# Performance work log

Hardware: AMD Instinct MI355X
Metric: run time of the kernel (lower is better)

The kernel has to match this reference:

```python
import jax, jax.numpy as jnp
import numpy as np

H = 1024      # hidden_size
I = 2048      # intermediate_size
E = 32        # num_routed_experts
B, S = 4, 2048


def setup_inputs() -> dict:
    key = jax.random.key(0)
    ks = jax.random.split(key, 8)
    scale = 0.02
    inp = {
        "hidden_states": jax.random.normal(ks[0], (B, S, H), dtype=jnp.float32),
        # router gate: stored [H, E] so logits = x @ gate_w
        "gate_w": jax.random.normal(ks[1], (H, E), dtype=jnp.float32) * scale,
        # shared SwiGLU (num_shared_experts=1), weights stored [in, out]
        "shared_gate_w": jax.random.normal(ks[2], (H, I), dtype=jnp.float32) * scale,
        "shared_up_w": jax.random.normal(ks[3], (H, I), dtype=jnp.float32) * scale,
        "shared_down_w": jax.random.normal(ks[4], (I, H), dtype=jnp.float32) * scale,
        # routed grouped SwiGLU, weights stored [E, in, out] (matches GroupedLinear)
        "routed_gate_w": jax.random.normal(ks[5], (E, H, I), dtype=jnp.float32) * scale,
        "routed_up_w": jax.random.normal(ks[6], (E, H, I), dtype=jnp.float32) * scale,
        "routed_down_w": jax.random.normal(ks[7], (E, I, H), dtype=jnp.float32) * scale,
    }
    return inp


def _grouped_mm(a, w, group_sizes):
    # a: [T, in], w: [E, in, out], group_sizes: [E] int32 -> [T, out]
    return jax.lax.ragged_dot(a, w, group_sizes)


def _swiglu(x, gw, uw, dw):
    return (jax.nn.silu(x @ gw) * (x @ uw)) @ dw


def reference(hidden_states, gate_w, shared_gate_w, shared_up_w, shared_down_w,
              routed_gate_w, routed_up_w, routed_down_w):
    b, s, h = hidden_states.shape
    x = hidden_states.reshape(-1, h)                      # [T, H]

    # ---- shared expert ----
    shared_out = _swiglu(x, shared_gate_w, shared_up_w, shared_down_w)

    # ---- router: top-1 ----
    logits = x @ gate_w                                   # [T, E]
    topk_ids = jnp.argmax(logits, axis=-1)                # [T]
    topk_val = jnp.max(logits, axis=-1)                   # [T]
    scores = jax.nn.sigmoid(topk_val)[:, None]            # [T, 1]
    xs = x * scores                                       # scale tokens by router score

    # ---- dispatch: sort tokens by expert id ----
    tokens_per_expert = jnp.zeros((E,), jnp.int32).at[topk_ids].add(1)
    order = jnp.argsort(topk_ids)                         # token ids sorted by expert
    sorted_x = xs[order]                                  # [T, H]

    # ---- grouped SwiGLU experts ----
    g = _grouped_mm(sorted_x, routed_gate_w, tokens_per_expert)   # [T, I]
    u = _grouped_mm(sorted_x, routed_up_w, tokens_per_expert)     # [T, I]
    d = _grouped_mm(jax.nn.silu(g) * u, routed_down_w, tokens_per_expert)  # [T, H]

    # ---- combine: unsort back to token order ----
    inv = jnp.argsort(order)
    routed_out = d[inv]

    return (shared_out + routed_out).reshape(b, s, h)
```

## Files before the change

### kernel.cpp

```cpp
#include <hip/hip_runtime.h>
#include <stdint.h>
#include <stddef.h>

#define TOK 8192
#define H 1024
#define IDIM 2048
#define NE 32
#define BM 128
#define BK 64
#define MAX_TILES 96

typedef __attribute__((ext_vector_type(8))) short short8;
typedef __attribute__((ext_vector_type(4))) float f32x4;
typedef __attribute__((ext_vector_type(4))) float float4v;
typedef __attribute__((ext_vector_type(4))) unsigned int uint4v;


__device__ __forceinline__ unsigned short f2bf(float x) {
  unsigned u = __builtin_bit_cast(unsigned, x);
  u += 0x7fffu + ((u >> 16) & 1u);
  return (unsigned short)(u >> 16);
}

__device__ __forceinline__ unsigned cvtpk(float lo, float hi) {
  unsigned r;
  asm("v_cvt_pk_bf16_f32 %0, %1, %2" : "=v"(r) : "v"(lo), "v"(hi));
  return r;
}

__device__ __forceinline__ void gll16(const void* g, void* l) {
  __builtin_amdgcn_global_load_lds(
      (const __attribute__((address_space(1))) unsigned int*)g,
      (__attribute__((address_space(3))) unsigned int*)l, 16, 0, 0);
}

__device__ __forceinline__ f32x4 mfma16(short8 a, short8 b, f32x4 c) {
  return __builtin_amdgcn_mfma_f32_16x16x32_bf16(a, b, c, 0, 0, 0);
}


__global__ __launch_bounds__(256) void tconv_kernel(
    const float* __restrict__ src0, unsigned short* __restrict__ dst0,
    int K, int N)
{
  __shared__ float t[64][65];
  const size_t mat = (size_t)K * N;
  const float* src = src0 + (size_t)blockIdx.z * mat;
  unsigned short* dst = dst0 + (size_t)blockIdx.z * mat;
  const int k0 = blockIdx.x * 64, n0 = blockIdx.y * 64;
  const int tid = threadIdx.x;
  {
    const int r = tid >> 4;
    const int c = (tid & 15) * 4;
    #pragma unroll
    for (int i = 0; i < 4; ++i) {
      float4v v = *(const float4v*)(src + (size_t)(k0 + r + i * 16) * N + (n0 + c));
      t[r + i * 16][c + 0] = v[0];
      t[r + i * 16][c + 1] = v[1];
      t[r + i * 16][c + 2] = v[2];
      t[r + i * 16][c + 3] = v[3];
    }
  }
  __syncthreads();
  {
    const int n = tid >> 2;
    const int kc = (tid & 3) * 16;
    uint4v o0, o1;
    #pragma unroll
    for (int q = 0; q < 4; ++q) {
      o0[q] = cvtpk(t[kc + 2 * q][n],     t[kc + 2 * q + 1][n]);
      o1[q] = cvtpk(t[kc + 8 + 2 * q][n], t[kc + 8 + 2 * q + 1][n]);
    }
    unsigned short* dp = dst + (size_t)(n0 + n) * K + (k0 + kc);
    *(uint4v*)dp = o0;
    *(uint4v*)(dp + 8) = o1;
  }
}


__global__ __launch_bounds__(256) void router_kernel(
    const float* __restrict__ x, const float* __restrict__ gw,
    unsigned short* __restrict__ xbf, unsigned short* __restrict__ xsbf,
    int* __restrict__ expert_id, int* __restrict__ counts)
{
  __shared__ float xl[8 * H];
  __shared__ float plog[8][8][NE];
  __shared__ float sscore[8];
  const int tid = threadIdx.x;
  const long t0 = (long)blockIdx.x * 8;

  const float4v* src = (const float4v*)(x + t0 * H);
  float4v* dst = (float4v*)xl;
  #pragma unroll
  for (int i = 0; i < 8; ++i) dst[tid + i * 256] = src[tid + i * 256];
  __syncthreads();

  {
    const int e = tid & 31, c = tid >> 5;
    float acc[8] = {0, 0, 0, 0, 0, 0, 0, 0};
    const float* gp = gw + (c * 128) * NE + e;
    for (int h = 0; h < 128; ++h) {
      float g = gp[h * NE];
      const float* xr = xl + (c * 128 + h);
      #pragma unroll
      for (int tk = 0; tk < 8; ++tk) acc[tk] += xr[tk * H] * g;
    }
    #pragma unroll
    for (int tk = 0; tk < 8; ++tk) plog[c][tk][e] = acc[tk];
  }
  __syncthreads();
  {
    const int e = tid & 31, tok = tid >> 5;
    float lg = 0.f;
    #pragma unroll
    for (int c = 0; c < 8; ++c) lg += plog[c][tok][e];
    float m = lg; int be = e;
    #pragma unroll
    for (int mask = 16; mask >= 1; mask >>= 1) {
      float om = __shfl_xor(m, mask);
      int   oe = __shfl_xor(be, mask);
      if (om > m || (om == m && oe < be)) { m = om; be = oe; }
    }
    if (e == 0) {
      sscore[tok] = 1.f / (1.f + __expf(-m));
      expert_id[t0 + tok] = be;
      atomicAdd(&counts[be], 1);
    }
  }
  __syncthreads();
  {
    const float sc = sscore[tid >> 5];
    const int base = (tid >> 5) * H + (tid & 31) * 32;
    #pragma unroll
    for (int i = 0; i < 4; ++i) {
      uint4v vx, vs;
      #pragma unroll
      for (int q = 0; q < 4; ++q) {
        const float a = xl[base + i * 8 + 2 * q];
        const float b = xl[base + i * 8 + 2 * q + 1];
        vx[q] = cvtpk(a, b);
        vs[q] = cvtpk(a * sc, b * sc);
      }
      *(uint4v*)(xbf  + t0 * H + base + i * 8) = vx;
      *(uint4v*)(xsbf + t0 * H + base + i * 8) = vs;
    }
  }
}


__global__ void scan_kernel(const int* __restrict__ counts, int* __restrict__ offsets,
                            int* __restrict__ cursor, int* __restrict__ tile_e,
                            int* __restrict__ tile_p, int* __restrict__ n_tiles)
{
  if (threadIdx.x != 0) return;
  int off = 0, nt = 0;
  for (int e = 0; e < NE; ++e) {
    offsets[e] = off; cursor[e] = off;
    int cc = counts[e];
    for (int k = 0; k < cc; k += BM) { tile_e[nt] = e; tile_p[nt] = off + k; ++nt; }
    off += cc;
  }
  offsets[NE] = off;
  n_tiles[0] = nt;
}


__global__ __launch_bounds__(256) void perm_kernel(
    const int* __restrict__ expert_id, int* __restrict__ cursor, int* __restrict__ perm)
{
  int t = blockIdx.x * 256 + threadIdx.x;
  int e = expert_id[t];
  int pos = atomicAdd(&cursor[e], 1);
  perm[pos] = t;
}


__global__ __launch_bounds__(256, 2) void gu_kernel(
    const unsigned short* __restrict__ xbf,
    const unsigned short* __restrict__ xsbf,
    const unsigned short* __restrict__ SG, const unsigned short* __restrict__ SU,
    const unsigned short* __restrict__ RG, const unsigned short* __restrict__ RU,
    unsigned short* __restrict__ act_sh, unsigned short* __restrict__ act_rt,
    const int* __restrict__ perm, const int* __restrict__ tile_e,
    const int* __restrict__ tile_p, const int* __restrict__ offsets,
    const int* __restrict__ n_tiles)
{
  __shared__ short Al[BM * BK];
  __shared__ short Gl[128 * BK];
  __shared__ short Ul[128 * BK];

  const int tid = threadIdx.x;
  const int wave = tid >> 6, lane = tid & 63;
  const int wm = wave >> 1, wn = wave & 1;

  const int bidx = blockIdx.y;
  const bool routed = bidx >= (TOK / BM);
  int row0, row_end;
  const unsigned short *Gt, *Ut, *A;
  unsigned short* act;
  if (routed) {
    const int tx = bidx - TOK / BM;
    if (tx >= *n_tiles) return;
    const int e = tile_e[tx];
    row0 = tile_p[tx];
    row_end = offsets[e + 1];
    Gt = RG + (size_t)e * H * IDIM;
    Ut = RU + (size_t)e * H * IDIM;
    A = xsbf; act = act_rt;
  } else {
    row0 = bidx * BM; row_end = row0 + BM;
    Gt = SG; Ut = SU;
    A = xbf; act = act_sh;
  }
  const int n0 = blockIdx.x * 128;

  const unsigned short *asrc[4], *gsrc[4], *usrc[4];
  int soff[4];
  #pragma unroll
  for (int i = 0; i < 4; ++i) {
    const int r = wave * 32 + i * 8 + (lane >> 3);
    int p = row0 + r;
    if (routed && p >= row_end) p = row0;
    const int arow = routed ? perm[p] : p;
    const int cb = ((lane & 7) * 16) ^ ((r & 7) << 4);
    asrc[i] = A  + (size_t)arow * H + (cb >> 1);
    gsrc[i] = Gt + (size_t)(n0 + r) * H + (cb >> 1);
    usrc[i] = Ut + (size_t)(n0 + r) * H + (cb >> 1);
    soff[i] = (wave * 32 + i * 8) * BK;
  }

  f32x4 accg[4][4] = {};
  f32x4 accu[4][4] = {};

  #pragma unroll 1
  for (int kt = 0; kt < H / BK; ++kt) {
    __syncthreads();
    #pragma unroll
    for (int i = 0; i < 4; ++i) gll16(asrc[i] + kt * BK, Al + soff[i]);
    #pragma unroll
    for (int i = 0; i < 4; ++i) gll16(gsrc[i] + kt * BK, Gl + soff[i]);
    #pragma unroll
    for (int i = 0; i < 4; ++i) gll16(usrc[i] + kt * BK, Ul + soff[i]);
    __syncthreads();

    #pragma unroll
    for (int kk = 0; kk < 2; ++kk) {
      short8 af[4];
      #pragma unroll
      for (int m = 0; m < 4; ++m) {
        const int r = wm * 64 + m * 16 + (lane & 15);
        const int cb = (kk * 64 + ((lane >> 4) * 16)) ^ ((r & 7) << 4);
        af[m] = *(const short8*)((const char*)Al + r * 128 + cb);
      }
      #pragma unroll
      for (int nf = 0; nf < 4; ++nf) {
        const int n = wn * 64 + nf * 16 + (lane & 15);
        const int cb = (kk * 64 + ((lane >> 4) * 16)) ^ ((n & 7) << 4);
        short8 bg = *(const short8*)((const char*)Gl + n * 128 + cb);
        short8 bu = *(const short8*)((const char*)Ul + n * 128 + cb);
        #pragma unroll
        for (int m = 0; m < 4; ++m) {
          accg[m][nf] = mfma16(af[m], bg, accg[m][nf]);
          accu[m][nf] = mfma16(af[m], bu, accu[m][nf]);
        }
      }
    }
  }

  #pragma unroll
  for (int m = 0; m < 4; ++m)
    #pragma unroll
    for (int nf = 0; nf < 4; ++nf) {
      const int col = n0 + wn * 64 + nf * 16 + (lane & 15);
      #pragma unroll
      for (int j = 0; j < 4; ++j) {
        const int row = row0 + wm * 64 + m * 16 + ((lane >> 4) * 4) + j;
        if (routed && row >= row_end) continue;
        const float g = accg[m][nf][j];
        const float u = accu[m][nf][j];
        const float v = (g / (1.f + __expf(-g))) * u;
        act[(size_t)row * IDIM + col] = f2bf(v);
      }
    }
}


template<bool ROUTED>
__global__ __launch_bounds__(256, 4) void dn_kernel(
    const unsigned short* __restrict__ A,
    const unsigned short* __restrict__ DT,
    float* __restrict__ out,
    const int* __restrict__ perm, const int* __restrict__ tile_e,
    const int* __restrict__ tile_p, const int* __restrict__ offsets,
    const int* __restrict__ n_tiles)
{
  __shared__ short Al[BM * BK];
  __shared__ short Dl[128 * BK];

  const int tid = threadIdx.x;
  const int wave = tid >> 6, lane = tid & 63;
  const int wm = wave >> 1, wn = wave & 1;

  int row0, row_end;
  const unsigned short* Dt;
  if constexpr (ROUTED) {
    if ((int)blockIdx.y >= *n_tiles) return;
    const int e = tile_e[blockIdx.y];
    row0 = tile_p[blockIdx.y];
    row_end = offsets[e + 1];
    Dt = DT + (size_t)e * H * IDIM;
  } else {
    row0 = blockIdx.y * BM; row_end = row0 + BM;
    Dt = DT;
  }
  const int n0 = blockIdx.x * 128;

  const unsigned short *asrc[4], *dsrc[4];
  int soff[4];
  #pragma unroll
  for (int i = 0; i < 4; ++i) {
    const int r = wave * 32 + i * 8 + (lane >> 3);
    int p = row0 + r;
    if (ROUTED && p >= row_end) p = row0;
    const int cb = ((lane & 7) * 16) ^ ((r & 7) << 4);
    asrc[i] = A  + (size_t)p * IDIM + (cb >> 1);
    dsrc[i] = Dt + (size_t)(n0 + r) * IDIM + (cb >> 1);
    soff[i] = (wave * 32 + i * 8) * BK;
  }

  f32x4 acc[4][4] = {};

  #pragma unroll 1
  for (int kt = 0; kt < IDIM / BK; ++kt) {
    __syncthreads();
    #pragma unroll
    for (int i = 0; i < 4; ++i) gll16(asrc[i] + kt * BK, Al + soff[i]);
    #pragma unroll
    for (int i = 0; i < 4; ++i) gll16(dsrc[i] + kt * BK, Dl + soff[i]);
    __syncthreads();

    #pragma unroll
    for (int kk = 0; kk < 2; ++kk) {
      short8 af[4];
      #pragma unroll
      for (int m = 0; m < 4; ++m) {
        const int r = wm * 64 + m * 16 + (lane & 15);
        const int cb = (kk * 64 + ((lane >> 4) * 16)) ^ ((r & 7) << 4);
        af[m] = *(const short8*)((const char*)Al + r * 128 + cb);
      }
      #pragma unroll
      for (int nf = 0; nf < 4; ++nf) {
        const int n = wn * 64 + nf * 16 + (lane & 15);
        const int cb = (kk * 64 + ((lane >> 4) * 16)) ^ ((n & 7) << 4);
        short8 bd = *(const short8*)((const char*)Dl + n * 128 + cb);
        #pragma unroll
        for (int m = 0; m < 4; ++m) acc[m][nf] = mfma16(af[m], bd, acc[m][nf]);
      }
    }
  }

  #pragma unroll
  for (int m = 0; m < 4; ++m)
    #pragma unroll
    for (int nf = 0; nf < 4; ++nf) {
      const int col = n0 + wn * 64 + nf * 16 + (lane & 15);
      #pragma unroll
      for (int j = 0; j < 4; ++j) {
        const int row = row0 + wm * 64 + m * 16 + ((lane >> 4) * 4) + j;
        const float v = acc[m][nf][j];
        if constexpr (ROUTED) {
          if (row < row_end) {
            const int t = perm[row];
            out[(size_t)t * H + col] += v;
          }
        } else {
          out[(size_t)row * H + col] = v;
        }
      }
    }
}


extern "C" void kernel_launch(void* const* d_in, const int* in_sizes, int n_in,
                              void* d_out, int out_size, void* d_ws, size_t ws_size,
                              hipStream_t stream) {
  (void)in_sizes; (void)n_in; (void)out_size; (void)ws_size;
  const float* x      = (const float*)d_in[0];
  const float* gate_w = (const float*)d_in[1];
  const float* sgw    = (const float*)d_in[2];
  const float* suw    = (const float*)d_in[3];
  const float* sdw    = (const float*)d_in[4];
  const float* rgw    = (const float*)d_in[5];
  const float* ruw    = (const float*)d_in[6];
  const float* rdw    = (const float*)d_in[7];
  float* out = (float*)d_out;

  char* ws = (char*)d_ws;
  unsigned short* xbf    = (unsigned short*)(ws + 0);
  unsigned short* xsbf   = (unsigned short*)(ws + 16777216);
  unsigned short* act_sh = (unsigned short*)(ws + 33554432);
  int* perm      = (int*)(ws + 67108864);
  int* expert_id = (int*)(ws + 67141632);
  int* counts    = (int*)(ws + 67174400);
  int* offsets   = (int*)(ws + 67174528);
  int* cursor    = (int*)(ws + 67174784);
  int* tile_e    = (int*)(ws + 67174912);
  int* tile_p    = (int*)(ws + 67175424);
  int* n_tiles   = (int*)(ws + 67175936);
  unsigned short* rgwT   = (unsigned short*)(ws + 68157440);
  unsigned short* ruwT   = (unsigned short*)(ws + 202375168);
  unsigned short* rdwT   = (unsigned short*)(ws + 336592896);
  unsigned short* sgwT   = (unsigned short*)(ws + 470810624);
  unsigned short* suwT   = (unsigned short*)(ws + 475004928);
  unsigned short* sdwT   = (unsigned short*)(ws + 479199232);
  unsigned short* act_rt = (unsigned short*)(ws + 483393536);

  hipMemsetAsync(counts, 0, NE * sizeof(int), stream);

  router_kernel<<<TOK / 8, 256, 0, stream>>>(x, gate_w, xbf, xsbf, expert_id, counts);
  scan_kernel<<<1, 64, 0, stream>>>(counts, offsets, cursor, tile_e, tile_p, n_tiles);
  perm_kernel<<<TOK / 256, 256, 0, stream>>>(expert_id, cursor, perm);

  tconv_kernel<<<dim3(H / 64, IDIM / 64, 1), 256, 0, stream>>>(sgw, sgwT, H, IDIM);
  tconv_kernel<<<dim3(H / 64, IDIM / 64, 1), 256, 0, stream>>>(suw, suwT, H, IDIM);
  tconv_kernel<<<dim3(H / 64, IDIM / 64, NE), 256, 0, stream>>>(rgw, rgwT, H, IDIM);
  tconv_kernel<<<dim3(H / 64, IDIM / 64, NE), 256, 0, stream>>>(ruw, ruwT, H, IDIM);
  gu_kernel<<<dim3(IDIM / 128, TOK / BM + MAX_TILES), 256, 0, stream>>>(
      xbf, xsbf, sgwT, suwT, rgwT, ruwT, act_sh, act_rt,
      perm, tile_e, tile_p, offsets, n_tiles);

  tconv_kernel<<<dim3(IDIM / 64, H / 64, 1), 256, 0, stream>>>(sdw, sdwT, IDIM, H);
  tconv_kernel<<<dim3(IDIM / 64, H / 64, NE), 256, 0, stream>>>(rdw, rdwT, IDIM, H);
  dn_kernel<false><<<dim3(H / 128, TOK / BM), 256, 0, stream>>>(
      act_sh, sdwT, out, perm, tile_e, tile_p, offsets, n_tiles);
  dn_kernel<true><<<dim3(H / 128, MAX_TILES), 256, 0, stream>>>(
      act_rt, rdwT, out, perm, tile_e, tile_p, offsets, n_tiles);
}
```

Before: 651.7 us.

## Fuse down-projection weight conversion into gate/up GEMM kernel grid

The two launches that transpose and convert the shared and routed down-projection weights to bf16 are folded into the gate/up GEMM kernel as extra trailing blocks. Those blocks reuse the kernel's shared memory and exit early, so the memory-bound conversion can overlap the compute-bound GEMM tail and two launches disappear. In exchange the GEMM kernel gains a branch and a unified 48KB shared buffer, which could affect occupancy or scheduling order.

```diff
diff --git a/kernel.cpp b/kernel.cpp
--- a/kernel.cpp
+++ b/kernel.cpp
@@ -9,6 +9,8 @@
 #define BM 128
 #define BK 64
 #define MAX_TILES 96
+#define GUTILES (TOK / BM + MAX_TILES)
+#define DNCONV_TILES 16896
 
 typedef __attribute__((ext_vector_type(8))) short short8;
 typedef __attribute__((ext_vector_type(4))) float f32x4;
@@ -38,17 +40,11 @@
   return __builtin_amdgcn_mfma_f32_16x16x32_bf16(a, b, c, 0, 0, 0);
 }
 
-
-__global__ __launch_bounds__(256) void tconv_kernel(
-    const float* __restrict__ src0, unsigned short* __restrict__ dst0,
-    int K, int N)
-{
-  __shared__ float t[64][65];
-  const size_t mat = (size_t)K * N;
-  const float* src = src0 + (size_t)blockIdx.z * mat;
-  unsigned short* dst = dst0 + (size_t)blockIdx.z * mat;
-  const int k0 = blockIdx.x * 64, n0 = blockIdx.y * 64;
-  const int tid = threadIdx.x;
+__device__ __forceinline__ void tconv_tile(
+    const float* __restrict__ src, unsigned short* __restrict__ dst,
+    int K, int N, int k0, int n0, int tid, void* smem)
+{
+  float (*t)[65] = (float(*)[65])smem;
   {
     const int r = tid >> 4;
     const int c = (tid & 15) * 4;
@@ -75,6 +71,17 @@
     *(uint4v*)dp = o0;
     *(uint4v*)(dp + 8) = o1;
   }
+}
+
+
+__global__ __launch_bounds__(256) void tconv_kernel(
+    const float* __restrict__ src0, unsigned short* __restrict__ dst0,
+    int K, int N)
+{
+  __shared__ float t[64][65];
+  const size_t mat = (size_t)K * N;
+  tconv_tile(src0 + (size_t)blockIdx.z * mat, dst0 + (size_t)blockIdx.z * mat,
+             K, N, blockIdx.x * 64, blockIdx.y * 64, threadIdx.x, t);
 }
 
 
@@ -181,25 +188,49 @@
     const unsigned short* __restrict__ SG, const unsigned short* __restrict__ SU,
     const unsigned short* __restrict__ RG, const unsigned short* __restrict__ RU,
     unsigned short* __restrict__ act_sh, unsigned short* __restrict__ act_rt,
+    const float* __restrict__ SDW, const float* __restrict__ RDW,
+    unsigned short* __restrict__ SDT, unsigned short* __restrict__ RDT,
     const int* __restrict__ perm, const int* __restrict__ tile_e,
     const int* __restrict__ tile_p, const int* __restrict__ offsets,
     const int* __restrict__ n_tiles)
 {
-  __shared__ short Al[BM * BK];
-  __shared__ short Gl[128 * BK];
-  __shared__ short Ul[128 * BK];
+  __shared__ char smem[49152];
 
   const int tid = threadIdx.x;
+  const int bidy = blockIdx.y;
+
+  if (bidy >= GUTILES) {
+    const int flat = (bidy - GUTILES) * (int)gridDim.x + (int)blockIdx.x;
+    const float* src;
+    unsigned short* dst;
+    int rem;
+    if (flat < 512 * NE) {
+      const int e = flat >> 9;
+      rem = flat & 511;
+      src = RDW + (size_t)e * IDIM * H;
+      dst = RDT + (size_t)e * IDIM * H;
+    } else {
+      rem = flat - 512 * NE;
+      src = SDW;
+      dst = SDT;
+    }
+    tconv_tile(src, dst, IDIM, H, (rem >> 4) * 64, (rem & 15) * 64, tid, smem);
+    return;
+  }
+
+  short* Al = (short*)smem;
+  short* Gl = Al + BM * BK;
+  short* Ul = Gl + 128 * BK;
+
   const int wave = tid >> 6, lane = tid & 63;
   const int wm = wave >> 1, wn = wave & 1;
 
-  const int bidx = blockIdx.y;
-  const bool routed = bidx >= (TOK / BM);
+  const bool routed = bidy >= (TOK / BM);
   int row0, row_end;
   const unsigned short *Gt, *Ut, *A;
   unsigned short* act;
   if (routed) {
-    const int tx = bidx - TOK / BM;
+    const int tx = bidy - TOK / BM;
     if (tx >= *n_tiles) return;
     const int e = tile_e[tx];
     row0 = tile_p[tx];
@@ -208,7 +239,7 @@
     Ut = RU + (size_t)e * H * IDIM;
     A = xsbf; act = act_rt;
   } else {
-    row0 = bidx * BM; row_end = row0 + BM;
+    row0 = bidy * BM; row_end = row0 + BM;
     Gt = SG; Ut = SU;
     A = xbf; act = act_sh;
   }
@@ -425,12 +456,11 @@
   tconv_kernel<<<dim3(H / 64, IDIM / 64, 1), 256, 0, stream>>>(suw, suwT, H, IDIM);
   tconv_kernel<<<dim3(H / 64, IDIM / 64, NE), 256, 0, stream>>>(rgw, rgwT, H, IDIM);
   tconv_kernel<<<dim3(H / 64, IDIM / 64, NE), 256, 0, stream>>>(ruw, ruwT, H, IDIM);
-  gu_kernel<<<dim3(IDIM / 128, TOK / BM + MAX_TILES), 256, 0, stream>>>(
+  gu_kernel<<<dim3(IDIM / 128, GUTILES + DNCONV_TILES / (IDIM / 128)), 256, 0, stream>>>(
       xbf, xsbf, sgwT, suwT, rgwT, ruwT, act_sh, act_rt,
+      sdw, rdw, sdwT, rdwT,
       perm, tile_e, tile_p, offsets, n_tiles);
 
-  tconv_kernel<<<dim3(IDIM / 64, H / 64, 1), 256, 0, stream>>>(sdw, sdwT, IDIM, H);
-  tconv_kernel<<<dim3(IDIM / 64, H / 64, NE), 256, 0, stream>>>(rdw, rdwT, IDIM, H);
   dn_kernel<false><<<dim3(H / 128, TOK / BM), 256, 0, stream>>>(
       act_sh, sdwT, out, perm, tile_e, tile_p, offsets, n_tiles);
   dn_kernel<true><<<dim3(H / 128, MAX_TILES), 256, 0, stream>>>(
```

Result: faster. 624.0 us (-4.3%).
